# Kernel optimization log

Hardware: AMD Instinct MI355X
Metric: run time of the kernel (lower is better)

Reference implementation:

```python
import jax, jax.numpy as jnp
import numpy as np

BITS = 4
MAXQ = 15            # 2**BITS - 1
PACK = 32 // BITS    # 8 int4 values per int32
GROUPSIZE = 128
M, K, N = 2048, 4096, 4096
G = K // GROUPSIZE


def setup_inputs() -> dict:
    key = jax.random.key(0)
    k1, k2, k3, k4, k5 = jax.random.split(key, 5)
    x = jax.random.normal(k1, (M, K), dtype=jnp.float32)
    qweight = jax.random.randint(k2, (K // PACK, N), 0, 2147483647, dtype=jnp.int32)
    qzeros = jax.random.randint(k3, (G, N // PACK), 0, 2147483647, dtype=jnp.int32)
    scales = jax.random.uniform(k4, (G, N), dtype=jnp.float32) * 0.01
    g_idx = (jnp.arange(K, dtype=jnp.int32) // GROUPSIZE).astype(jnp.int32)
    bias = jax.random.normal(k5, (N,), dtype=jnp.float32)
    return {"x": x, "qweight": qweight, "qzeros": qzeros,
            "scales": scales, "g_idx": g_idx, "bias": bias}


def _dequantize(qweight, qzeros, scales, g_idx):
    shifts = (jnp.arange(PACK, dtype=jnp.int32) * BITS)
    # unpack weights along K: [K//8, N] -> [K//8, 8, N] -> [K, N]
    w_int = ((qweight[:, None, :] >> shifts[None, :, None]) & MAXQ)
    w_int = w_int.reshape(K, N)
    # unpack zeros along N: [G, N//8] -> [G, N//8, 8] -> [G, N]; kernel adds 1
    z_int = ((qzeros[:, :, None] >> shifts[None, None, :]) & MAXQ) + 1
    z_int = z_int.reshape(G, N)
    # group-wise dequant: W[k, n] = (w - zeros[g_idx[k]]) * scales[g_idx[k]]
    W = (w_int - z_int[g_idx]).astype(jnp.float32) * scales[g_idx]
    return W  # [K, N]


def reference(x, qweight, qzeros, scales, g_idx, bias):
    W = _dequantize(qweight, qzeros, scales, g_idx)
    return x @ W + bias  # [M, N]
```

## Files before the change

### kernel.cpp

```cpp
#include <hip/hip_runtime.h>
#include <hip/hip_bf16.h>
#include <stdint.h>

#define M_DIM 2048
#define K_DIM 4096
#define N_DIM 4096

typedef __attribute__((ext_vector_type(8))) short short8;
typedef __attribute__((ext_vector_type(4))) float f32x4;

__device__ __forceinline__ uint32_t bf16pk(float a, float b) {
  uint32_t ua = __float_as_uint(a);
  ua = (ua + 0x7FFFu + ((ua >> 16) & 1u)) >> 16;
  uint32_t ub = __float_as_uint(b);
  ub = (ub + 0x7FFFu + ((ub >> 16) & 1u)) >> 16;
  return ua | (ub << 16);
}

__global__ void __launch_bounds__(256) cvt_x_kernel(const float* __restrict__ x,
                                                    uint32_t* __restrict__ xImg) {
  int bid = blockIdx.x;
  int mt = bid >> 6;
  int kt = bid & 63;
  int tid = threadIdx.x;
  uint32_t* tileOut = xImg + (size_t)(mt * 64 + kt) * 4096;
  const float* xbase = x + (size_t)mt * 128 * K_DIM + kt * 64;
#pragma unroll
  for (int i = 0; i < 4; ++i) {
    int o = i * 256 + tid;
    int m = o >> 3;
    int slot = o & 7;
    int k8 = slot ^ (m & 7);
    const float* src = xbase + (size_t)m * K_DIM + k8 * 8;
    float4 f0 = *(const float4*)(src);
    float4 f1 = *(const float4*)(src + 4);
    uint4 pk;
    pk.x = bf16pk(f0.x, f0.y);
    pk.y = bf16pk(f0.z, f0.w);
    pk.z = bf16pk(f1.x, f1.y);
    pk.w = bf16pk(f1.z, f1.w);
    *(uint4*)(tileOut + (size_t)o * 4) = pk;
  }
}

__global__ void __launch_bounds__(256) deq_w_kernel(const uint32_t* __restrict__ qweight,
                                                    const uint32_t* __restrict__ qzeros,
                                                    const float* __restrict__ scales,
                                                    uint32_t* __restrict__ wImg) {
  __shared__ uint32_t img[4096];
  int bid = blockIdx.x;
  int kt = bid & 63;
  int nt = bid >> 6;
  int tid = threadIdx.x;
  int n = tid & 127;
  int kh = tid >> 7;
  int g = kt >> 1;
  int gn = nt * 128 + n;

  uint32_t zq = qzeros[g * (N_DIM / 8) + (gn >> 3)];
  int z = (int)((zq >> ((gn & 7) * 4)) & 15u) + 1;
  float s = scales[g * N_DIM + gn];

#pragma unroll
  for (int j = 0; j < 4; ++j) {
    int k8 = kh * 4 + j;
    uint32_t q = qweight[(size_t)(kt * 8 + k8) * N_DIM + gn];
    float f[8];
#pragma unroll
    for (int v = 0; v < 8; ++v) {
      int w = (int)((q >> (4 * v)) & 15u);
      f[v] = (float)(w - z) * s;
    }
    uint4 pk;
    pk.x = bf16pk(f[0], f[1]);
    pk.y = bf16pk(f[2], f[3]);
    pk.z = bf16pk(f[4], f[5]);
    pk.w = bf16pk(f[6], f[7]);
    int slot = k8 ^ (n & 7);
    *(uint4*)(&img[(n * 8 + slot) * 4]) = pk;
  }
  __syncthreads();
  uint32_t* tileOut = wImg + (size_t)(nt * 64 + kt) * 4096;
#pragma unroll
  for (int i = 0; i < 4; ++i) {
    int o = i * 256 + tid;
    *(uint4*)(tileOut + (size_t)o * 4) = *(const uint4*)(&img[o * 4]);
  }
}

__global__ void __launch_bounds__(256) gemm_kernel(const uint32_t* __restrict__ xImg,
                                                   const uint32_t* __restrict__ wImg,
                                                   const float* __restrict__ bias,
                                                   float* __restrict__ out) {
  __shared__ uint32_t sA[4096];
  __shared__ uint32_t sB[4096];
  int bid = blockIdx.x;
  int nb = bid & 31;
  int mb = bid >> 5;
  int tid = threadIdx.x;
  int lane = tid & 63;
  int wid = tid >> 6;
  int wr = wid >> 1, wc = wid & 1;
  int lr = lane & 15, lk = lane >> 4;

  f32x4 acc[4][4];
#pragma unroll
  for (int i = 0; i < 4; ++i)
#pragma unroll
    for (int j = 0; j < 4; ++j) acc[i][j] = f32x4{0.f, 0.f, 0.f, 0.f};

  const char* aTile = (const char*)(xImg + (size_t)mb * 64 * 4096);
  const char* bTile = (const char*)(wImg + (size_t)nb * 64 * 4096);

  int swz = (lr & 7) << 4;
  int rowA[4], rowB[4];
#pragma unroll
  for (int i = 0; i < 4; ++i) rowA[i] = (wr * 64 + i * 16 + lr) * 128;
#pragma unroll
  for (int j = 0; j < 4; ++j) rowB[j] = (wc * 64 + j * 16 + lr) * 128;

  for (int kt = 0; kt < 64; ++kt) {
#pragma unroll
    for (int s2 = 0; s2 < 4; ++s2) {
      int c = wid * 4 + s2;
      int off = c * 1024 + lane * 16;
      __builtin_amdgcn_global_load_lds(
          (__attribute__((address_space(1))) void*)(aTile + off),
          (__attribute__((address_space(3))) void*)((char*)sA + c * 1024), 16, 0, 0);
      __builtin_amdgcn_global_load_lds(
          (__attribute__((address_space(1))) void*)(bTile + off),
          (__attribute__((address_space(3))) void*)((char*)sB + c * 1024), 16, 0, 0);
    }
    __syncthreads();
#pragma unroll
    for (int ks = 0; ks < 2; ++ks) {
      int kb = ks * 64 + lk * 16;
      int ko = kb ^ swz;
      short8 af[4], bf[4];
#pragma unroll
      for (int i = 0; i < 4; ++i)
        af[i] = *(const short8*)((const char*)sA + rowA[i] + ko);
#pragma unroll
      for (int j = 0; j < 4; ++j)
        bf[j] = *(const short8*)((const char*)sB + rowB[j] + ko);
#pragma unroll
      for (int i = 0; i < 4; ++i)
#pragma unroll
        for (int j = 0; j < 4; ++j)
          acc[i][j] = __builtin_amdgcn_mfma_f32_16x16x32_bf16(af[i], bf[j], acc[i][j], 0, 0, 0);
    }
    __syncthreads();
    aTile += 16384;
    bTile += 16384;
  }

  int colBase = nb * 128 + wc * 64 + lr;
  int rowBase = mb * 128 + wr * 64 + lk * 4;
#pragma unroll
  for (int j = 0; j < 4; ++j) {
    int col = colBase + j * 16;
    float bj = bias[col];
#pragma unroll
    for (int i = 0; i < 4; ++i) {
      int row = rowBase + i * 16;
#pragma unroll
      for (int r = 0; r < 4; ++r) {
        out[(size_t)(row + r) * N_DIM + col] = acc[i][j][r] + bj;
      }
    }
  }
}

__global__ void fallback_kernel(const float* __restrict__ x, const uint32_t* __restrict__ qweight,
                                const uint32_t* __restrict__ qzeros, const float* __restrict__ scales,
                                const float* __restrict__ bias, float* __restrict__ out) {
  __shared__ float xs[16][17];
  __shared__ float ws[16][17];
  int tx = threadIdx.x, ty = threadIdx.y;
  int col = blockIdx.x * 16 + tx;
  int row = blockIdx.y * 16 + ty;
  float acc = 0.f;
  for (int k0 = 0; k0 < K_DIM; k0 += 16) {
    xs[ty][tx] = x[(size_t)row * K_DIM + k0 + tx];
    int k = k0 + ty;
    int g = k >> 7;
    uint32_t q = qweight[(size_t)(k >> 3) * N_DIM + col];
    int w = (int)((q >> ((k & 7) * 4)) & 15u);
    uint32_t zq = qzeros[g * (N_DIM / 8) + (col >> 3)];
    int z = (int)((zq >> ((col & 7) * 4)) & 15u) + 1;
    ws[ty][tx] = (float)(w - z) * scales[g * N_DIM + col];
    __syncthreads();
#pragma unroll
    for (int kk = 0; kk < 16; ++kk) acc += xs[ty][kk] * ws[kk][tx];
    __syncthreads();
  }
  out[(size_t)row * N_DIM + col] = acc + bias[col];
}

extern "C" void kernel_launch(void* const* d_in, const int* in_sizes, int n_in,
                              void* d_out, int out_size, void* d_ws, size_t ws_size,
                              hipStream_t stream) {
  const float* x = (const float*)d_in[0];
  const uint32_t* qweight = (const uint32_t*)d_in[1];
  const uint32_t* qzeros = (const uint32_t*)d_in[2];
  const float* scales = (const float*)d_in[3];
  const float* bias = (const float*)d_in[5];
  float* out = (float*)d_out;

  const size_t X_IMG_BYTES = (size_t)16 * 64 * 16384;
  const size_t W_IMG_BYTES = (size_t)32 * 64 * 16384;

  if (ws_size >= X_IMG_BYTES + W_IMG_BYTES) {
    uint32_t* xImg = (uint32_t*)d_ws;
    uint32_t* wImg = (uint32_t*)((char*)d_ws + X_IMG_BYTES);
    cvt_x_kernel<<<1024, 256, 0, stream>>>(x, xImg);
    deq_w_kernel<<<2048, 256, 0, stream>>>(qweight, qzeros, scales, wImg);
    gemm_kernel<<<512, 256, 0, stream>>>(xImg, wImg, bias, out);
  } else {
    fallback_kernel<<<dim3(N_DIM / 16, M_DIM / 16), dim3(16, 16), 0, stream>>>(
        x, qweight, qzeros, scales, bias, out);
  }
}
```

Measured before the change: 97.92 us.

## Rework GEMM with split-K, 3-stage LDS pipeline, new tile layouts and atomics

The GEMM now uses 128x256 output tiles with a two-way split-K whose partial sums are combined through float atomicAdd into an output zeroed by a memset, and block indices are remapped across XCDs. Global-to-LDS loads run through a three-buffer pipeline with explicit vmcnt waits, and MFMA issue is wrapped in setprio. The x-conversion and weight-dequant kernels write new k-major tile images, with the x path transposed through LDS. This targets better load/compute overlap and fewer barriers, at the cost of atomic traffic, an extra memset and nondeterministic summation order.

Result: slower. 146.4 us (+49.6%).

```diff
diff --git a/kernel.cpp b/kernel.cpp
--- a/kernel.cpp
+++ b/kernel.cpp
@@ -17,54 +17,53 @@
   return ua | (ub << 16);
 }
 
+__device__ __forceinline__ void glds16(const char* g, char* l) {
+  __builtin_amdgcn_global_load_lds((__attribute__((address_space(1))) void*)g,
+                                   (__attribute__((address_space(3))) void*)l, 16, 0, 0);
+}
+
+
 __global__ void __launch_bounds__(256) cvt_x_kernel(const float* __restrict__ x,
-                                                    uint32_t* __restrict__ xImg) {
-  int bid = blockIdx.x;
-  int mt = bid >> 6;
-  int kt = bid & 63;
-  int tid = threadIdx.x;
-  uint32_t* tileOut = xImg + (size_t)(mt * 64 + kt) * 4096;
-  const float* xbase = x + (size_t)mt * 128 * K_DIM + kt * 64;
-#pragma unroll
-  for (int i = 0; i < 4; ++i) {
+                                                    char* __restrict__ xImg) {
+  __shared__ char lds[128 * 528];
+  const int mt = blockIdx.x >> 4, ktG = blockIdx.x & 15;
+  const int tid = threadIdx.x;
+  const float* xb = x + (size_t)mt * 128 * K_DIM + ktG * 256;
+#pragma unroll
+  for (int i = 0; i < 32; ++i) {
+    int idx = i * 256 + tid;
+    int row = idx >> 6, c4 = idx & 63;
+    float4 f = *(const float4*)(xb + (size_t)row * K_DIM + c4 * 4);
+    uint2 pk;
+    pk.x = bf16pk(f.x, f.y);
+    pk.y = bf16pk(f.z, f.w);
+    *(uint2*)(lds + row * 528 + c4 * 8) = pk;
+  }
+  __syncthreads();
+  char* outb = xImg + (size_t)(mt * 128 + ktG * 8) * 8192;
+#pragma unroll
+  for (int i = 0; i < 16; ++i) {
     int o = i * 256 + tid;
-    int m = o >> 3;
-    int slot = o & 7;
-    int k8 = slot ^ (m & 7);
-    const float* src = xbase + (size_t)m * K_DIM + k8 * 8;
-    float4 f0 = *(const float4*)(src);
-    float4 f1 = *(const float4*)(src + 4);
-    uint4 pk;
-    pk.x = bf16pk(f0.x, f0.y);
-    pk.y = bf16pk(f0.z, f0.w);
-    pk.z = bf16pk(f1.x, f1.y);
-    pk.w = bf16pk(f1.z, f1.w);
-    *(uint4*)(tileOut + (size_t)o * 4) = pk;
+    int tile = o >> 9, r = o & 511, slot = r >> 7, m = r & 127;
+    uint4 v = *(const uint4*)(lds + m * 528 + tile * 64 + slot * 16);
+    *(uint4*)(outb + (size_t)tile * 8192 + slot * 2048 + m * 16) = v;
   }
 }
 
 __global__ void __launch_bounds__(256) deq_w_kernel(const uint32_t* __restrict__ qweight,
                                                     const uint32_t* __restrict__ qzeros,
                                                     const float* __restrict__ scales,
-                                                    uint32_t* __restrict__ wImg) {
-  __shared__ uint32_t img[4096];
-  int bid = blockIdx.x;
-  int kt = bid & 63;
-  int nt = bid >> 6;
-  int tid = threadIdx.x;
-  int n = tid & 127;
-  int kh = tid >> 7;
-  int g = kt >> 1;
-  int gn = nt * 128 + n;
-
-  uint32_t zq = qzeros[g * (N_DIM / 8) + (gn >> 3)];
-  int z = (int)((zq >> ((gn & 7) * 4)) & 15u) + 1;
-  float s = scales[g * N_DIM + gn];
-
-#pragma unroll
-  for (int j = 0; j < 4; ++j) {
-    int k8 = kh * 4 + j;
-    uint32_t q = qweight[(size_t)(kt * 8 + k8) * N_DIM + gn];
+                                                    char* __restrict__ wImg) {
+  const int nt8 = blockIdx.x >> 5, g = blockIdx.x & 31;
+  const int t = threadIdx.x;
+  const int ng = nt8 * 256 + t;
+  uint32_t zq = qzeros[g * (N_DIM / 8) + (ng >> 3)];
+  const int z = (int)((zq >> ((ng & 7) * 4)) & 15u) + 1;
+  const float s = scales[g * N_DIM + ng];
+  char* base = wImg + (size_t)nt8 * 128 * 16384;
+#pragma unroll
+  for (int i = 0; i < 16; ++i) {
+    uint32_t q = qweight[(size_t)(g * 16 + i) * N_DIM + ng];
     float f[8];
 #pragma unroll
     for (int v = 0; v < 8; ++v) {
@@ -76,97 +75,92 @@
     pk.y = bf16pk(f[2], f[3]);
     pk.z = bf16pk(f[4], f[5]);
     pk.w = bf16pk(f[6], f[7]);
-    int slot = k8 ^ (n & 7);
-    *(uint4*)(&img[(n * 8 + slot) * 4]) = pk;
-  }
-  __syncthreads();
-  uint32_t* tileOut = wImg + (size_t)(nt * 64 + kt) * 4096;
-#pragma unroll
-  for (int i = 0; i < 4; ++i) {
-    int o = i * 256 + tid;
-    *(uint4*)(tileOut + (size_t)o * 4) = *(const uint4*)(&img[o * 4]);
-  }
-}
-
-__global__ void __launch_bounds__(256) gemm_kernel(const uint32_t* __restrict__ xImg,
-                                                   const uint32_t* __restrict__ wImg,
-                                                   const float* __restrict__ bias,
-                                                   float* __restrict__ out) {
-  __shared__ uint32_t sA[4096];
-  __shared__ uint32_t sB[4096];
-  int bid = blockIdx.x;
-  int nb = bid & 31;
-  int mb = bid >> 5;
-  int tid = threadIdx.x;
-  int lane = tid & 63;
-  int wid = tid >> 6;
-  int wr = wid >> 1, wc = wid & 1;
-  int lr = lane & 15, lk = lane >> 4;
-
-  f32x4 acc[4][4];
-#pragma unroll
-  for (int i = 0; i < 4; ++i)
+    int kt32 = g * 4 + (i >> 2), slot = i & 3;
+    *(uint4*)(base + (size_t)kt32 * 16384 + slot * 4096 + t * 16) = pk;
+  }
+}
+
+__global__ void __launch_bounds__(256, 2) gemm_kernel(const char* __restrict__ xImg,
+                                                      const char* __restrict__ wImg,
+                                                      const float* __restrict__ bias,
+                                                      float* __restrict__ out) {
+  __shared__ char lds[73728];
+  const int b = blockIdx.x;
+  const int wg = (b & 7) * 64 + (b >> 3);
+  const int mb = wg >> 5, ks = (wg >> 4) & 1, nb = wg & 15;
+  const int tid = threadIdx.x, lane = tid & 63, wc = tid >> 6;
+  const int lr = lane & 15, lk = lane >> 4;
+
+  f32x4 acc[8][4];
+#pragma unroll
+  for (int i = 0; i < 8; ++i)
 #pragma unroll
     for (int j = 0; j < 4; ++j) acc[i][j] = f32x4{0.f, 0.f, 0.f, 0.f};
 
-  const char* aTile = (const char*)(xImg + (size_t)mb * 64 * 4096);
-  const char* bTile = (const char*)(wImg + (size_t)nb * 64 * 4096);
-
-  int swz = (lr & 7) << 4;
-  int rowA[4], rowB[4];
-#pragma unroll
-  for (int i = 0; i < 4; ++i) rowA[i] = (wr * 64 + i * 16 + lr) * 128;
-#pragma unroll
-  for (int j = 0; j < 4; ++j) rowB[j] = (wc * 64 + j * 16 + lr) * 128;
-
-  for (int kt = 0; kt < 64; ++kt) {
-#pragma unroll
-    for (int s2 = 0; s2 < 4; ++s2) {
-      int c = wid * 4 + s2;
-      int off = c * 1024 + lane * 16;
-      __builtin_amdgcn_global_load_lds(
-          (__attribute__((address_space(1))) void*)(aTile + off),
-          (__attribute__((address_space(3))) void*)((char*)sA + c * 1024), 16, 0, 0);
-      __builtin_amdgcn_global_load_lds(
-          (__attribute__((address_space(1))) void*)(bTile + off),
-          (__attribute__((address_space(3))) void*)((char*)sB + c * 1024), 16, 0, 0);
+  const char* aT = xImg + (size_t)(mb * 128 + ks * 64) * 8192;
+  const char* bT = wImg + (size_t)(nb * 128 + ks * 64) * 16384;
+
+  int aoff[8], boff[4];
+#pragma unroll
+  for (int i = 0; i < 8; ++i) aoff[i] = lk * 2048 + (i * 16 + lr) * 16;
+#pragma unroll
+  for (int j = 0; j < 4; ++j) boff[j] = 8192 + lk * 4096 + (wc * 64 + j * 16 + lr) * 16;
+
+#define STAGE(T, C)                                                          \
+  do {                                                                       \
+    char* dA = lds + (C) * 24576;                                            \
+    const char* sA = aT + (size_t)(T) * 8192;                                \
+    const char* sB = bT + (size_t)(T) * 16384;                               \
+    glds16(sA + tid * 16, dA + tid * 16);                                    \
+    glds16(sA + 4096 + tid * 16, dA + 4096 + tid * 16);                      \
+    glds16(sB + tid * 16, dA + 8192 + tid * 16);                             \
+    glds16(sB + 4096 + tid * 16, dA + 12288 + tid * 16);                     \
+    glds16(sB + 8192 + tid * 16, dA + 16384 + tid * 16);                     \
+    glds16(sB + 12288 + tid * 16, dA + 20480 + tid * 16);                    \
+  } while (0)
+
+  STAGE(0, 0);
+  STAGE(1, 1);
+
+  int c = 0;
+  for (int t = 0; t < 64; ++t) {
+    if (t < 63) asm volatile("s_waitcnt vmcnt(6)" ::: "memory");
+    else        asm volatile("s_waitcnt vmcnt(0)" ::: "memory");
+    __builtin_amdgcn_sched_barrier(0);
+    __builtin_amdgcn_s_barrier();
+    if (t < 62) {
+      int cn = c + 2; if (cn >= 3) cn -= 3;
+      STAGE(t + 2, cn);
     }
-    __syncthreads();
-#pragma unroll
-    for (int ks = 0; ks < 2; ++ks) {
-      int kb = ks * 64 + lk * 16;
-      int ko = kb ^ swz;
-      short8 af[4], bf[4];
-#pragma unroll
-      for (int i = 0; i < 4; ++i)
-        af[i] = *(const short8*)((const char*)sA + rowA[i] + ko);
+    const char* buf = lds + c * 24576;
+    short8 af[8], bf[4];
+#pragma unroll
+    for (int i = 0; i < 8; ++i) af[i] = *(const short8*)(buf + aoff[i]);
+#pragma unroll
+    for (int j = 0; j < 4; ++j) bf[j] = *(const short8*)(buf + boff[j]);
+    __builtin_amdgcn_s_setprio(1);
+#pragma unroll
+    for (int i = 0; i < 8; ++i)
 #pragma unroll
       for (int j = 0; j < 4; ++j)
-        bf[j] = *(const short8*)((const char*)sB + rowB[j] + ko);
-#pragma unroll
-      for (int i = 0; i < 4; ++i)
-#pragma unroll
-        for (int j = 0; j < 4; ++j)
-          acc[i][j] = __builtin_amdgcn_mfma_f32_16x16x32_bf16(af[i], bf[j], acc[i][j], 0, 0, 0);
-    }
-    __syncthreads();
-    aTile += 16384;
-    bTile += 16384;
-  }
-
-  int colBase = nb * 128 + wc * 64 + lr;
-  int rowBase = mb * 128 + wr * 64 + lk * 4;
+        acc[i][j] = __builtin_amdgcn_mfma_f32_16x16x32_bf16(af[i], bf[j], acc[i][j], 0, 0, 0);
+    __builtin_amdgcn_s_setprio(0);
+    c = (c == 2) ? 0 : c + 1;
+  }
+#undef STAGE
+
+  const int colB = nb * 256 + wc * 64 + lr;
+  const int rowB = mb * 128 + lk * 4;
 #pragma unroll
   for (int j = 0; j < 4; ++j) {
-    int col = colBase + j * 16;
-    float bj = bias[col];
-#pragma unroll
-    for (int i = 0; i < 4; ++i) {
-      int row = rowBase + i * 16;
-#pragma unroll
-      for (int r = 0; r < 4; ++r) {
-        out[(size_t)(row + r) * N_DIM + col] = acc[i][j][r] + bj;
-      }
+    int col = colB + j * 16;
+    float bj = (ks == 0) ? bias[col] : 0.f;
+#pragma unroll
+    for (int i = 0; i < 8; ++i) {
+      int row = rowB + i * 16;
+#pragma unroll
+      for (int r = 0; r < 4; ++r)
+        atomicAdd(&out[(size_t)(row + r) * N_DIM + col], acc[i][j][r] + bj);
     }
   }
 }
@@ -207,14 +201,15 @@
   const float* bias = (const float*)d_in[5];
   float* out = (float*)d_out;
 
-  const size_t X_IMG_BYTES = (size_t)16 * 64 * 16384;
-  const size_t W_IMG_BYTES = (size_t)32 * 64 * 16384;
+  const size_t X_IMG_BYTES = (size_t)16 * 128 * 8192;
+  const size_t W_IMG_BYTES = (size_t)16 * 128 * 16384;
 
   if (ws_size >= X_IMG_BYTES + W_IMG_BYTES) {
-    uint32_t* xImg = (uint32_t*)d_ws;
-    uint32_t* wImg = (uint32_t*)((char*)d_ws + X_IMG_BYTES);
-    cvt_x_kernel<<<1024, 256, 0, stream>>>(x, xImg);
-    deq_w_kernel<<<2048, 256, 0, stream>>>(qweight, qzeros, scales, wImg);
+    char* xImg = (char*)d_ws;
+    char* wImg = (char*)d_ws + X_IMG_BYTES;
+    hipMemsetAsync(out, 0, (size_t)M_DIM * N_DIM * sizeof(float), stream);
+    cvt_x_kernel<<<256, 256, 0, stream>>>(x, xImg);
+    deq_w_kernel<<<512, 256, 0, stream>>>(qweight, qzeros, scales, wImg);
     gemm_kernel<<<512, 256, 0, stream>>>(xImg, wImg, bias, out);
   } else {
     fallback_kernel<<<dim3(N_DIM / 16, M_DIM / 16), dim3(16, 16), 0, stream>>>(
```
